# Performance work log

Hardware: AMD Instinct MI355X
Metric: run time of the kernel (lower is better)

Reference implementation:

```python
import jax, jax.numpy as jnp
import numpy as np

B, T, I, H, O, TGT = 64, 512, 64, 512, 64, 96
SCALE = 0.05


def setup_inputs() -> dict:
    key = jax.random.key(0)
    ks = jax.random.split(key, 12)
    rn = lambda k, sh: jax.random.normal(k, sh, jnp.float32) * SCALE
    return {
        "x": jax.random.normal(ks[0], (B, T, I), jnp.float32),
        "W_ih0": rn(ks[1], (4 * H, I)),
        "W_hh0": rn(ks[2], (4 * H, H)),
        "b_ih0": rn(ks[3], (4 * H,)),
        "b_hh0": rn(ks[4], (4 * H,)),
        "W_ih1": rn(ks[5], (4 * H, H)),
        "W_hh1": rn(ks[6], (4 * H, H)),
        "b_ih1": rn(ks[7], (4 * H,)),
        "b_hh1": rn(ks[8], (4 * H,)),
        "W_fc": rn(ks[9], (O, H)),
        "b_fc": rn(ks[10], (O,)),
        "target_len": TGT,
    }


def _cell(x_t, h, c, Wi, Wh, b):
    # PyTorch LSTM gate order: i, f, g, o
    g = x_t @ Wi.T + h @ Wh.T + b  # [B, 4H]
    i, f, gg, o = jnp.split(g, 4, axis=-1)
    c_new = jax.nn.sigmoid(f) * c + jax.nn.sigmoid(i) * jnp.tanh(gg)
    h_new = jax.nn.sigmoid(o) * jnp.tanh(c_new)
    return h_new, c_new


def _run_layer(seq_tbf, Wi, Wh, b):
    # seq_tbf: [T, B, F]; returns hidden sequence [T, B, H] and final (h, c)
    nb = seq_tbf.shape[1]
    hdim = Wh.shape[1]
    init = (jnp.zeros((nb, hdim), seq_tbf.dtype), jnp.zeros((nb, hdim), seq_tbf.dtype))

    def step(carry, x_t):
        h, c = _cell(x_t, carry[0], carry[1], Wi, Wh, b)
        return (h, c), h

    (h, c), hs = jax.lax.scan(step, init, seq_tbf)
    return hs, h, c


def reference(x, W_ih0, W_hh0, b_ih0, b_hh0, W_ih1, W_hh1, b_ih1, b_hh1, W_fc, b_fc, target_len):
    # Dropout is inactive (eval-mode reference).
    b0 = b_ih0 + b_hh0
    b1 = b_ih1 + b_hh1

    # --- encoder pass over full context ---
    seq = jnp.transpose(x, (1, 0, 2))                 # [T, B, I]
    hs0, h0, c0 = _run_layer(seq, W_ih0, W_hh0, b0)   # layer 0
    _, h1, c1 = _run_layer(hs0, W_ih1, W_hh1, b1)     # layer 1

    x_in = x[:, -1, :]  # [B, I]

    def dec_step(carry, _):
        h0, c0, h1, c1, xi = carry
        h0, c0 = _cell(xi, h0, c0, W_ih0, W_hh0, b0)
        h1, c1 = _cell(h0, h1, c1, W_ih1, W_hh1, b1)
        y = h1 @ W_fc.T + b_fc  # [B, O], fed back as next input
        return (h0, c0, h1, c1, y), y

    _, ys = jax.lax.scan(dec_step, (h0, c0, h1, c1, x_in), None, length=target_len)
    return jnp.transpose(ys, (1, 0, 2))  # [B, target_len, O]
```

## Files before the change

kernel.cpp:

```cpp
#include <hip/hip_runtime.h>
#include <stdint.h>


#define NWG 256
#define NTH 256

constexpr int Tt = 512, TGT = 96;

typedef __attribute__((ext_vector_type(8))) short bf16x8;
typedef __attribute__((ext_vector_type(4))) float f32x4;
typedef unsigned long long u64;

__device__ __forceinline__ unsigned short f2bf(float f) {
  union { float f; unsigned u; } v; v.f = f;
  return (unsigned short)((v.u + 0x7fffu + ((v.u >> 16) & 1u)) >> 16);
}
__device__ __forceinline__ float bf2f(unsigned short h) {
  union { unsigned u; float f; } v; v.u = ((unsigned)h) << 16; return v.f;
}
__device__ __forceinline__ float sigm(float x) { return 1.f / (1.f + __expf(-x)); }
__device__ __forceinline__ float tanh_(float x) { return 1.f - 2.f / (__expf(2.f * x) + 1.f); }

__device__ __forceinline__ unsigned ald32a(const unsigned* p) {
  return __hip_atomic_load(p, __ATOMIC_RELAXED, __HIP_MEMORY_SCOPE_AGENT);
}
__device__ __forceinline__ void ast32a(unsigned* p, unsigned v) {
  __hip_atomic_store(p, v, __ATOMIC_RELAXED, __HIP_MEMORY_SCOPE_AGENT);
}
__device__ __forceinline__ u64 ald64a(const u64* p) {
  return __hip_atomic_load(p, __ATOMIC_RELAXED, __HIP_MEMORY_SCOPE_AGENT);
}
__device__ __forceinline__ void ast64a(u64* p, u64 v) {
  __hip_atomic_store(p, v, __ATOMIC_RELAXED, __HIP_MEMORY_SCOPE_AGENT);
}

struct SMem {
  unsigned short wB[2][4][16][64][8];
  u64 a0[16 * 68];
  u64 a1[16 * 68];
  unsigned short wfc2[1024];
  float gpart[4][272];
  float fcp[256];
  float b0s[64], b1s[64], b0d[64], bfc2[2];
};

__device__ __forceinline__ int amap(int idx) {
  int b = idx >> 7, k8 = idx & 127;
  return (k8 >> 3) * 68 + b * 8 + (k8 & 7);
}

__device__ __forceinline__ void stage1(u64* dst, const u64* src, int tid) {
  u64 v0 = ald64a(src + tid),       v1 = ald64a(src + tid + 256);
  u64 v2 = ald64a(src + tid + 512), v3 = ald64a(src + tid + 768);
  dst[amap(tid)] = v0; dst[amap(tid + 256)] = v1;
  dst[amap(tid + 512)] = v2; dst[amap(tid + 768)] = v3;
}
__device__ __forceinline__ void stage2(u64* d0, const u64* s0, u64* d1, const u64* s1, int tid) {
  u64 v0 = ald64a(s0 + tid),       v1 = ald64a(s0 + tid + 256);
  u64 v2 = ald64a(s0 + tid + 512), v3 = ald64a(s0 + tid + 768);
  u64 v4 = ald64a(s1 + tid),       v5 = ald64a(s1 + tid + 256);
  u64 v6 = ald64a(s1 + tid + 512), v7 = ald64a(s1 + tid + 768);
  d0[amap(tid)] = v0; d0[amap(tid + 256)] = v1;
  d0[amap(tid + 512)] = v2; d0[amap(tid + 768)] = v3;
  d1[amap(tid)] = v4; d1[amap(tid + 256)] = v5;
  d1[amap(tid + 512)] = v6; d1[amap(tid + 768)] = v7;
}

__device__ __forceinline__ void gbar(unsigned* slots, int g, int w, unsigned tgt) {
  __syncthreads();
  if (threadIdx.x == 0) ast32a(slots + g * 32 + w, tgt);
  if (threadIdx.x < 64) {
    const unsigned* sp = slots + g * 32 + (threadIdx.x & 31);
    while (true) {
      unsigned v = ald32a(sp);
      if (__all((int)(v >= tgt))) break;
      __builtin_amdgcn_s_sleep(1);
    }
  }
  __syncthreads();
}

#define MFMA(a, b, c) __builtin_amdgcn_mfma_f32_16x16x32_bf16(a, b, c, 0, 0, 0)

__global__ __launch_bounds__(NTH, 1) void lstm_kernel(
    const float* __restrict__ x,
    const float* __restrict__ Wih0, const float* __restrict__ Whh0,
    const float* __restrict__ bih0, const float* __restrict__ bhh0,
    const float* __restrict__ Wih1, const float* __restrict__ Whh1,
    const float* __restrict__ bih1, const float* __restrict__ bhh1,
    const float* __restrict__ Wfc, const float* __restrict__ bfc,
    u64* h0q, u64* h1q, unsigned* slots, float* __restrict__ out)
{
  __shared__ SMem sm;
  const int g = blockIdx.x & 7;
  const int wgw = blockIdx.x >> 3;
  const int tid = threadIdx.x;

  for (int e = tid; e < 8192; e += NTH) {
    int m = e >> 12, w4 = (e >> 10) & 3, kc = (e >> 6) & 15, l = e & 63;
    int colx = l & 15, qx = l >> 4;
    size_t row = (size_t)((colx & 3) * 512 + wgw * 16 + w4 * 4 + (colx >> 2));
    const float* src = (m ? Wih1 : Whh0) + row * 512 + kc * 32 + qx * 8;
    unsigned short* dst = &sm.wB[m][w4][kc][l][0];
    float4 u = *(const float4*)src, v = *(const float4*)(src + 4);
    dst[0] = f2bf(u.x); dst[1] = f2bf(u.y); dst[2] = f2bf(u.z); dst[3] = f2bf(u.w);
    dst[4] = f2bf(v.x); dst[5] = f2bf(v.y); dst[6] = f2bf(v.z); dst[7] = f2bf(v.w);
  }
  for (int e = tid; e < 1024; e += NTH)
    sm.wfc2[e] = f2bf(Wfc[(size_t)(wgw * 2 + (e >> 9)) * 512 + (e & 511)]);
  if (tid < 64) {
    int jj = tid >> 2, g4 = tid & 3;
    int grow = g4 * 512 + wgw * 16 + jj;
    float s0 = bih0[grow] + bhh0[grow];
    sm.b0s[tid] = s0;
    sm.b1s[tid] = bih1[grow] + bhh1[grow];
    float ex = 0.f;
    for (int i = 0; i < 64; ++i) ex += Wih0[(size_t)grow * 64 + i] * bfc[i];
    sm.b0d[tid] = s0 + ex;
  }
  if (tid < 2) sm.bfc2[tid] = bfc[wgw * 2 + tid];

  const int wave = tid >> 6, lane = tid & 63;
  const int col = lane & 15, quad = lane >> 4;
  const int koff = quad * 8;
  const size_t rowg = (size_t)((col & 3) * 512 + wgw * 16 + wave * 4 + (col >> 2));

  bf16x8 whh1f[16];
#pragma unroll
  for (int kc = 0; kc < 16; ++kc) {
    const float* p = Whh1 + rowg * 512 + kc * 32 + koff;
    float4 u = *(const float4*)p, v = *(const float4*)(p + 4);
    bf16x8 r;
    r[0] = (short)f2bf(u.x); r[1] = (short)f2bf(u.y); r[2] = (short)f2bf(u.z); r[3] = (short)f2bf(u.w);
    r[4] = (short)f2bf(v.x); r[5] = (short)f2bf(v.y); r[6] = (short)f2bf(v.z); r[7] = (short)f2bf(v.w);
    whh1f[kc] = r;
  }
  bf16x8 wih0f[2];
#pragma unroll
  for (int kc = 0; kc < 2; ++kc) {
    const float* p = Wih0 + rowg * 64 + kc * 32 + koff;
    float4 u = *(const float4*)p, v = *(const float4*)(p + 4);
    bf16x8 r;
    r[0] = (short)f2bf(u.x); r[1] = (short)f2bf(u.y); r[2] = (short)f2bf(u.z); r[3] = (short)f2bf(u.w);
    r[4] = (short)f2bf(v.x); r[5] = (short)f2bf(v.y); r[6] = (short)f2bf(v.z); r[7] = (short)f2bf(v.w);
    wih0f[kc] = r;
  }
  bf16x8 wcombf[16];
  {
    float wc[16][8];
#pragma unroll
    for (int kc = 0; kc < 16; ++kc)
#pragma unroll
      for (int j = 0; j < 8; ++j) wc[kc][j] = 0.f;
    for (int i = 0; i < 64; ++i) {
      float wi = Wih0[rowg * 64 + i];
      const float* fr = Wfc + (size_t)i * 512 + koff;
#pragma unroll
      for (int kc = 0; kc < 16; ++kc) {
        float4 u = *(const float4*)(fr + kc * 32);
        float4 v = *(const float4*)(fr + kc * 32 + 4);
        wc[kc][0] += wi * u.x; wc[kc][1] += wi * u.y;
        wc[kc][2] += wi * u.z; wc[kc][3] += wi * u.w;
        wc[kc][4] += wi * v.x; wc[kc][5] += wi * v.y;
        wc[kc][6] += wi * v.z; wc[kc][7] += wi * v.w;
      }
    }
#pragma unroll
    for (int kc = 0; kc < 16; ++kc) {
      bf16x8 r;
#pragma unroll
      for (int j = 0; j < 8; ++j) r[j] = (short)f2bf(wc[kc][j]);
      wcombf[kc] = r;
    }
  }
  __syncthreads();

  const float b0c = sm.b0s[wave * 16 + col];
  const float b1c = sm.b1s[wave * 16 + col];
  const float b0dc = sm.b0d[wave * 16 + col];
  const unsigned short* pw0 = &sm.wB[0][wave][0][lane][0];
  const unsigned short* pw1 = &sm.wB[1][wave][0][lane][0];
  const u64* afrag0 = sm.a0 + (col & 7) * 8 + quad * 2;
  const u64* afrag1 = sm.a1 + (col & 7) * 8 + quad * 2;
  unsigned ph = 0;
  float c0 = 0.f, c1 = 0.f;
  const size_t xstride = (size_t)Tt * 64;

  auto loadx = [&](const float* p) -> bf16x8 {
    float4 u = *(const float4*)p, v = *(const float4*)(p + 4);
    bf16x8 r;
    r[0] = (short)f2bf(u.x); r[1] = (short)f2bf(u.y); r[2] = (short)f2bf(u.z); r[3] = (short)f2bf(u.w);
    r[4] = (short)f2bf(v.x); r[5] = (short)f2bf(v.y); r[6] = (short)f2bf(v.z); r[7] = (short)f2bf(v.w);
    return r;
  };

  auto actstore = [&](f32x4 v, float& cst, u64* hdst) {
    float* gp = sm.gpart[wave];
#pragma unroll
    for (int r = 0; r < 4; ++r) gp[(quad * 4 + r) * 17 + col] = v[r];
    unsigned hbits = 0;
    int b = lane >> 2, j = lane & 3;
    if (lane < 32) {
      const float* ro = gp + b * 17 + j * 4;
      float iv = sigm(ro[0]), fv = sigm(ro[1]), gv = tanh_(ro[2]), ov = sigm(ro[3]);
      float c = fv * cst + iv * gv; cst = c;
      hbits = f2bf(ov * tanh_(c));
    }
    unsigned h1b = __shfl(hbits, (lane + 1) & 63);
    unsigned h2b = __shfl(hbits, (lane + 2) & 63);
    unsigned h3b = __shfl(hbits, (lane + 3) & 63);
    if (lane < 32 && j == 0) {
      u64 pk = (u64)hbits | ((u64)h1b << 16) | ((u64)h2b << 32) | ((u64)h3b << 48);
      ast64a(hdst + b * 128 + wgw * 4 + wave, pk);
    }
  };

  auto fcpart = [&](const u64* asrc) {
    int ks = tid >> 4, b = (tid >> 1) & 7, cc = tid & 1;
    const unsigned short* hr = (const unsigned short*)(asrc + ks * 68 + b * 8);
    const unsigned short* wp = sm.wfc2 + cc * 512 + ks * 32;
    float s = 0.f;
#pragma unroll
    for (int k2 = 0; k2 < 4; ++k2) {
      bf16x8 hv = *(const bf16x8*)(hr + k2 * 8);
      bf16x8 wv = *(const bf16x8*)(wp + k2 * 8);
#pragma unroll
      for (int q2 = 0; q2 < 8; ++q2) s += bf2f((unsigned short)hv[q2]) * bf2f((unsigned short)wv[q2]);
    }
    sm.fcp[tid] = s;
  };
  auto fcout = [&](int d) {
    if (tid < 16) {
      float sv = sm.bfc2[tid & 1];
#pragma unroll
      for (int k = 0; k < 16; ++k) sv += sm.fcp[k * 16 + tid];
      int bb = tid >> 1, cc = tid & 1;
      out[(size_t)(g * 8 + bb) * (TGT * 64) + d * 64 + (wgw * 2 + cc)] = sv;
    }
  };

  for (int t = 0; t <= Tt; ++t) {
    const u64* h0prev = h0q + ((t + 1) & 1) * 8192 + g * 1024;
    u64* h0cur = h0q + (t & 1) * 8192 + g * 1024;
    const u64* h1prev = h1q + (t & 1) * 8192 + g * 1024;
    u64* h1cur = h1q + ((t + 1) & 1) * 8192 + g * 1024;

    bf16x8 xa0, xa1;
    if (t < Tt) {
      const float* xb = x + (size_t)(g * 8 + (col & 7)) * xstride + (size_t)t * 64 + koff;
      xa0 = loadx(xb); xa1 = loadx(xb + 32);
    }
    if (t == 1)      { stage1(sm.a0, h0prev, tid); __syncthreads(); }
    else if (t >= 2) { stage2(sm.a0, h0prev, sm.a1, h1prev, tid); __syncthreads(); }

    if (t < Tt) {
      f32x4 za = {b0c, b0c, b0c, b0c}, zb = {0.f, 0.f, 0.f, 0.f};
      za = MFMA(xa0, wih0f[0], za);
      zb = MFMA(xa1, wih0f[1], zb);
      if (t >= 1) {
        f32x4 ya = {b1c, b1c, b1c, b1c}, yb = {0.f, 0.f, 0.f, 0.f};
#pragma unroll
        for (int kc = 0; kc < 16; ++kc) {
          bf16x8 a = *(const bf16x8*)(afrag0 + kc * 68);
          bf16x8 w0 = *(const bf16x8*)(pw0 + kc * 512);
          bf16x8 w1 = *(const bf16x8*)(pw1 + kc * 512);
          if (kc & 1) { zb = MFMA(a, w0, zb); yb = MFMA(a, w1, yb); }
          else        { za = MFMA(a, w0, za); ya = MFMA(a, w1, ya); }
        }
        if (t >= 2) {
#pragma unroll
          for (int kc = 0; kc < 16; ++kc) {
            bf16x8 a = *(const bf16x8*)(afrag1 + kc * 68);
            if (kc & 1) yb = MFMA(a, whh1f[kc], yb);
            else        ya = MFMA(a, whh1f[kc], ya);
          }
        }
        actstore(za + zb, c0, h0cur);
        actstore(ya + yb, c1, h1cur);
      } else {
        actstore(za + zb, c0, h0cur);
      }
    } else {
      f32x4 ya = {b1c, b1c, b1c, b1c}, yb = {0.f, 0.f, 0.f, 0.f};
#pragma unroll
      for (int kc = 0; kc < 16; ++kc) {
        bf16x8 a = *(const bf16x8*)(afrag0 + kc * 68);
        bf16x8 w1 = *(const bf16x8*)(pw1 + kc * 512);
        if (kc & 1) yb = MFMA(a, w1, yb);
        else        ya = MFMA(a, w1, ya);
      }
#pragma unroll
      for (int kc = 0; kc < 16; ++kc) {
        bf16x8 a = *(const bf16x8*)(afrag1 + kc * 68);
        if (kc & 1) yb = MFMA(a, whh1f[kc], yb);
        else        ya = MFMA(a, whh1f[kc], ya);
      }
      actstore(ya + yb, c1, h1cur);
    }
    gbar(slots, g, wgw, ++ph);
  }

  {
    stage2(sm.a0, h0q + 8192 + g * 1024, sm.a1, h1q + 8192 + g * 1024, tid);
    __syncthreads();
    const float* xb = x + (size_t)(g * 8 + (col & 7)) * xstride + (size_t)(Tt - 1) * 64 + koff;
    bf16x8 xa0 = loadx(xb), xa1 = loadx(xb + 32);
    f32x4 za = {b0c, b0c, b0c, b0c}, zb = {0.f, 0.f, 0.f, 0.f};
    za = MFMA(xa0, wih0f[0], za);
    zb = MFMA(xa1, wih0f[1], zb);
#pragma unroll
    for (int kc = 0; kc < 16; ++kc) {
      bf16x8 a = *(const bf16x8*)(afrag0 + kc * 68);
      bf16x8 w0 = *(const bf16x8*)(pw0 + kc * 512);
      if (kc & 1) zb = MFMA(a, w0, zb);
      else        za = MFMA(a, w0, za);
    }
    actstore(za + zb, c0, h0q + g * 1024);
  }
  gbar(slots, g, wgw, ++ph);
  {
    stage1(sm.a0, h0q + g * 1024, tid);
    __syncthreads();
    f32x4 ya = {b1c, b1c, b1c, b1c}, yb = {0.f, 0.f, 0.f, 0.f};
#pragma unroll
    for (int kc = 0; kc < 16; ++kc) {
      bf16x8 a = *(const bf16x8*)(afrag0 + kc * 68);
      bf16x8 w1 = *(const bf16x8*)(pw1 + kc * 512);
      bf16x8 a2 = *(const bf16x8*)(afrag1 + kc * 68);
      if (kc & 1) { yb = MFMA(a, w1, yb); yb = MFMA(a2, whh1f[kc], yb); }
      else        { ya = MFMA(a, w1, ya); ya = MFMA(a2, whh1f[kc], ya); }
    }
    actstore(ya + yb, c1, h1q + g * 1024);
  }
  gbar(slots, g, wgw, ++ph);

  for (int d = 1; d < TGT; ++d) {
    {
      stage2(sm.a0, h0q + ((d + 1) & 1) * 8192 + g * 1024,
             sm.a1, h1q + ((d + 1) & 1) * 8192 + g * 1024, tid);
      __syncthreads();
      fcpart(sm.a1);
      f32x4 za = {b0dc, b0dc, b0dc, b0dc}, zb = {0.f, 0.f, 0.f, 0.f};
#pragma unroll
      for (int kc = 0; kc < 16; ++kc) {
        bf16x8 a = *(const bf16x8*)(afrag0 + kc * 68);
        bf16x8 w0 = *(const bf16x8*)(pw0 + kc * 512);
        bf16x8 a2 = *(const bf16x8*)(afrag1 + kc * 68);
        if (kc & 1) { zb = MFMA(a, w0, zb); zb = MFMA(a2, wcombf[kc], zb); }
        else        { za = MFMA(a, w0, za); za = MFMA(a2, wcombf[kc], za); }
      }
      actstore(za + zb, c0, h0q + (d & 1) * 8192 + g * 1024);
      __syncthreads();
      fcout(d - 1);
    }
    gbar(slots, g, wgw, ++ph);

    {
      stage1(sm.a0, h0q + (d & 1) * 8192 + g * 1024, tid);
      __syncthreads();
      f32x4 ya = {b1c, b1c, b1c, b1c}, yb = {0.f, 0.f, 0.f, 0.f};
#pragma unroll
      for (int kc = 0; kc < 16; ++kc) {
        bf16x8 a = *(const bf16x8*)(afrag0 + kc * 68);
        bf16x8 w1 = *(const bf16x8*)(pw1 + kc * 512);
        bf16x8 a2 = *(const bf16x8*)(afrag1 + kc * 68);
        if (kc & 1) { yb = MFMA(a, w1, yb); yb = MFMA(a2, whh1f[kc], yb); }
        else        { ya = MFMA(a, w1, ya); ya = MFMA(a2, whh1f[kc], ya); }
      }
      actstore(ya + yb, c1, h1q + (d & 1) * 8192 + g * 1024);
    }
    gbar(slots, g, wgw, ++ph);
  }

  {
    stage1(sm.a1, h1q + 8192 + g * 1024, tid);
    __syncthreads();
    fcpart(sm.a1);
    __syncthreads();
    fcout(TGT - 1);
  }
}

extern "C" void kernel_launch(void* const* d_in, const int* in_sizes, int n_in,
                              void* d_out, int out_size, void* d_ws, size_t ws_size,
                              hipStream_t stream) {
  (void)in_sizes; (void)n_in; (void)out_size; (void)ws_size;
  const float* x    = (const float*)d_in[0];
  const float* Wih0 = (const float*)d_in[1];
  const float* Whh0 = (const float*)d_in[2];
  const float* bih0 = (const float*)d_in[3];
  const float* bhh0 = (const float*)d_in[4];
  const float* Wih1 = (const float*)d_in[5];
  const float* Whh1 = (const float*)d_in[6];
  const float* bih1 = (const float*)d_in[7];
  const float* bhh1 = (const float*)d_in[8];
  const float* Wfc  = (const float*)d_in[9];
  const float* bfc  = (const float*)d_in[10];

  char* ws = (char*)d_ws;
  unsigned* slots = (unsigned*)ws;
  u64* h0q = (u64*)(ws + 2048);
  u64* h1q = (u64*)(ws + 2048 + 131072);

  hipMemsetAsync(slots, 0, 2048, stream);
  hipLaunchKernelGGL(lstm_kernel, dim3(NWG), dim3(NTH), 0, stream,
                     x, Wih0, Whh0, bih0, bhh0, Wih1, Whh1, bih1, bhh1, Wfc, bfc,
                     h0q, h1q, slots, (float*)d_out);
}
```

Before: 2.898 ms.

## Replace per-step global barriers with tag-bit polling on hidden-state data

Drops the slot-counter barrier that ran after every LSTM step. Each packed bf16 hidden value now carries an epoch-parity tag in its exponent MSB, and consumers spin on the data itself until every tag matches before staging it into LDS. This removes a separate flag write plus polling round trip per step and lets workgroups wait only on the data they actually need. The trade-off is that it relies on |h|<2 so the tag bit is otherwise zero, and a bounded retry guard could let stale data through if a producer is very late.

```diff
diff --git a/kernel.cpp b/kernel.cpp
--- a/kernel.cpp
+++ b/kernel.cpp
@@ -11,6 +11,8 @@
 typedef __attribute__((ext_vector_type(4))) float f32x4;
 typedef unsigned long long u64;
 
+#define TAGBITS 0x4000400040004000ULL
+
 __device__ __forceinline__ unsigned short f2bf(float f) {
   union { float f; unsigned u; } v; v.f = f;
   return (unsigned short)((v.u + 0x7fffu + ((v.u >> 16) & 1u)) >> 16);
@@ -21,17 +23,17 @@
 __device__ __forceinline__ float sigm(float x) { return 1.f / (1.f + __expf(-x)); }
 __device__ __forceinline__ float tanh_(float x) { return 1.f - 2.f / (__expf(2.f * x) + 1.f); }
 
-__device__ __forceinline__ unsigned ald32a(const unsigned* p) {
-  return __hip_atomic_load(p, __ATOMIC_RELAXED, __HIP_MEMORY_SCOPE_AGENT);
-}
-__device__ __forceinline__ void ast32a(unsigned* p, unsigned v) {
-  __hip_atomic_store(p, v, __ATOMIC_RELAXED, __HIP_MEMORY_SCOPE_AGENT);
-}
 __device__ __forceinline__ u64 ald64a(const u64* p) {
   return __hip_atomic_load(p, __ATOMIC_RELAXED, __HIP_MEMORY_SCOPE_AGENT);
 }
 __device__ __forceinline__ void ast64a(u64* p, u64 v) {
   __hip_atomic_store(p, v, __ATOMIC_RELAXED, __HIP_MEMORY_SCOPE_AGENT);
+}
+
+__device__ __forceinline__ u64 tmask(int e) {
+  int q = (e >> 1) & 3;
+  return (u64)(q & 1) * 0x0000400000004000ULL
+       | (u64)((q >> 1) & 1) * 0x4000000040000000ULL;
 }
 
 struct SMem {
@@ -49,35 +51,40 @@
   return (k8 >> 3) * 68 + b * 8 + (k8 & 7);
 }
 
-__device__ __forceinline__ void stage1(u64* dst, const u64* src, int tid) {
-  u64 v0 = ald64a(src + tid),       v1 = ald64a(src + tid + 256);
-  u64 v2 = ald64a(src + tid + 512), v3 = ald64a(src + tid + 768);
-  dst[amap(tid)] = v0; dst[amap(tid + 256)] = v1;
-  dst[amap(tid + 512)] = v2; dst[amap(tid + 768)] = v3;
-}
-__device__ __forceinline__ void stage2(u64* d0, const u64* s0, u64* d1, const u64* s1, int tid) {
-  u64 v0 = ald64a(s0 + tid),       v1 = ald64a(s0 + tid + 256);
-  u64 v2 = ald64a(s0 + tid + 512), v3 = ald64a(s0 + tid + 768);
-  u64 v4 = ald64a(s1 + tid),       v5 = ald64a(s1 + tid + 256);
-  u64 v6 = ald64a(s1 + tid + 512), v7 = ald64a(s1 + tid + 768);
-  d0[amap(tid)] = v0; d0[amap(tid + 256)] = v1;
-  d0[amap(tid + 512)] = v2; d0[amap(tid + 768)] = v3;
-  d1[amap(tid)] = v4; d1[amap(tid + 256)] = v5;
-  d1[amap(tid + 512)] = v6; d1[amap(tid + 768)] = v7;
-}
-
-__device__ __forceinline__ void gbar(unsigned* slots, int g, int w, unsigned tgt) {
-  __syncthreads();
-  if (threadIdx.x == 0) ast32a(slots + g * 32 + w, tgt);
-  if (threadIdx.x < 64) {
-    const unsigned* sp = slots + g * 32 + (threadIdx.x & 31);
-    while (true) {
-      unsigned v = ald32a(sp);
-      if (__all((int)(v >= tgt))) break;
-      __builtin_amdgcn_s_sleep(1);
-    }
-  }
-  __syncthreads();
+__device__ __forceinline__ void pollstage1(u64* dst, const u64* src, u64 want, int tid) {
+  u64 v0, v1, v2, v3;
+  int guard = 0;
+  while (true) {
+    v0 = ald64a(src + tid);       v1 = ald64a(src + tid + 256);
+    v2 = ald64a(src + tid + 512); v3 = ald64a(src + tid + 768);
+    bool ok = ((v0 & TAGBITS) == want) & ((v1 & TAGBITS) == want) &
+              ((v2 & TAGBITS) == want) & ((v3 & TAGBITS) == want);
+    if (ok || ++guard > 8192) break;
+    __builtin_amdgcn_s_sleep(1);
+  }
+  dst[amap(tid)]       = v0 & ~TAGBITS; dst[amap(tid + 256)] = v1 & ~TAGBITS;
+  dst[amap(tid + 512)] = v2 & ~TAGBITS; dst[amap(tid + 768)] = v3 & ~TAGBITS;
+}
+__device__ __forceinline__ void pollstage2(u64* d0, const u64* s0, u64 w0,
+                                           u64* d1, const u64* s1, u64 w1, int tid) {
+  u64 a0, a1, a2, a3, b0, b1, b2, b3;
+  int guard = 0;
+  while (true) {
+    a0 = ald64a(s0 + tid);       a1 = ald64a(s0 + tid + 256);
+    a2 = ald64a(s0 + tid + 512); a3 = ald64a(s0 + tid + 768);
+    b0 = ald64a(s1 + tid);       b1 = ald64a(s1 + tid + 256);
+    b2 = ald64a(s1 + tid + 512); b3 = ald64a(s1 + tid + 768);
+    bool ok = ((a0 & TAGBITS) == w0) & ((a1 & TAGBITS) == w0) &
+              ((a2 & TAGBITS) == w0) & ((a3 & TAGBITS) == w0) &
+              ((b0 & TAGBITS) == w1) & ((b1 & TAGBITS) == w1) &
+              ((b2 & TAGBITS) == w1) & ((b3 & TAGBITS) == w1);
+    if (ok || ++guard > 8192) break;
+    __builtin_amdgcn_s_sleep(1);
+  }
+  d0[amap(tid)]       = a0 & ~TAGBITS; d0[amap(tid + 256)] = a1 & ~TAGBITS;
+  d0[amap(tid + 512)] = a2 & ~TAGBITS; d0[amap(tid + 768)] = a3 & ~TAGBITS;
+  d1[amap(tid)]       = b0 & ~TAGBITS; d1[amap(tid + 256)] = b1 & ~TAGBITS;
+  d1[amap(tid + 512)] = b2 & ~TAGBITS; d1[amap(tid + 768)] = b3 & ~TAGBITS;
 }
 
 #define MFMA(a, b, c) __builtin_amdgcn_mfma_f32_16x16x32_bf16(a, b, c, 0, 0, 0)
@@ -89,7 +96,7 @@
     const float* __restrict__ Wih1, const float* __restrict__ Whh1,
     const float* __restrict__ bih1, const float* __restrict__ bhh1,
     const float* __restrict__ Wfc, const float* __restrict__ bfc,
-    u64* h0q, u64* h1q, unsigned* slots, float* __restrict__ out)
+    u64* h0q, u64* h1q, float* __restrict__ out)
 {
   __shared__ SMem sm;
   const int g = blockIdx.x & 7;
@@ -182,9 +189,12 @@
   const unsigned short* pw1 = &sm.wB[1][wave][0][lane][0];
   const u64* afrag0 = sm.a0 + (col & 7) * 8 + quad * 2;
   const u64* afrag1 = sm.a1 + (col & 7) * 8 + quad * 2;
-  unsigned ph = 0;
   float c0 = 0.f, c1 = 0.f;
   const size_t xstride = (size_t)Tt * 64;
+
+  auto hslot = [&](u64* hq, int e) -> u64* {
+    return hq + ((size_t)(e & 1) << 13) + g * 1024;
+  };
 
   auto loadx = [&](const float* p) -> bf16x8 {
     float4 u = *(const float4*)p, v = *(const float4*)(p + 4);
@@ -194,7 +204,7 @@
     return r;
   };
 
-  auto actstore = [&](f32x4 v, float& cst, u64* hdst) {
+  auto actstore = [&](f32x4 v, float& cst, u64* hdst, u64 tg) {
     float* gp = sm.gpart[wave];
 #pragma unroll
     for (int r = 0; r < 4; ++r) gp[(quad * 4 + r) * 17 + col] = v[r];
@@ -211,7 +221,7 @@
     unsigned h3b = __shfl(hbits, (lane + 3) & 63);
     if (lane < 32 && j == 0) {
       u64 pk = (u64)hbits | ((u64)h1b << 16) | ((u64)h2b << 32) | ((u64)h3b << 48);
-      ast64a(hdst + b * 128 + wgw * 4 + wave, pk);
+      ast64a(hdst + b * 128 + wgw * 4 + wave, pk | tg);
     }
   };
 
@@ -240,18 +250,21 @@
   };
 
   for (int t = 0; t <= Tt; ++t) {
-    const u64* h0prev = h0q + ((t + 1) & 1) * 8192 + g * 1024;
-    u64* h0cur = h0q + (t & 1) * 8192 + g * 1024;
-    const u64* h1prev = h1q + (t & 1) * 8192 + g * 1024;
-    u64* h1cur = h1q + ((t + 1) & 1) * 8192 + g * 1024;
-
     bf16x8 xa0, xa1;
     if (t < Tt) {
       const float* xb = x + (size_t)(g * 8 + (col & 7)) * xstride + (size_t)t * 64 + koff;
       xa0 = loadx(xb); xa1 = loadx(xb + 32);
     }
-    if (t == 1)      { stage1(sm.a0, h0prev, tid); __syncthreads(); }
-    else if (t >= 2) { stage2(sm.a0, h0prev, sm.a1, h1prev, tid); __syncthreads(); }
+    if (t == 1) {
+      __syncthreads();
+      pollstage1(sm.a0, hslot(h0q, 0), tmask(0), tid);
+      __syncthreads();
+    } else if (t >= 2) {
+      __syncthreads();
+      pollstage2(sm.a0, hslot(h0q, t - 1), tmask(t - 1),
+                 sm.a1, hslot(h1q, t - 2), tmask(t - 2), tid);
+      __syncthreads();
+    }
 
     if (t < Tt) {
       f32x4 za = {b0c, b0c, b0c, b0c}, zb = {0.f, 0.f, 0.f, 0.f};
@@ -275,10 +288,10 @@
             else        ya = MFMA(a, whh1f[kc], ya);
           }
         }
-        actstore(za + zb, c0, h0cur);
-        actstore(ya + yb, c1, h1cur);
+        actstore(za + zb, c0, hslot(h0q, t), tmask(t));
+        actstore(ya + yb, c1, hslot(h1q, t - 1), tmask(t - 1));
       } else {
-        actstore(za + zb, c0, h0cur);
+        actstore(za + zb, c0, hslot(h0q, 0), tmask(0));
       }
     } else {
       f32x4 ya = {b1c, b1c, b1c, b1c}, yb = {0.f, 0.f, 0.f, 0.f};
@@ -295,13 +308,14 @@
         if (kc & 1) yb = MFMA(a, whh1f[kc], yb);
         else        ya = MFMA(a, whh1f[kc], ya);
       }
-      actstore(ya + yb, c1, h1cur);
-    }
-    gbar(slots, g, wgw, ++ph);
+      actstore(ya + yb, c1, hslot(h1q, Tt - 1), tmask(Tt - 1));
+    }
   }
 
   {
-    stage2(sm.a0, h0q + 8192 + g * 1024, sm.a1, h1q + 8192 + g * 1024, tid);
+    __syncthreads();
+    pollstage2(sm.a0, hslot(h0q, 511), tmask(511),
+               sm.a1, hslot(h1q, 511), tmask(511), tid);
     __syncthreads();
     const float* xb = x + (size_t)(g * 8 + (col & 7)) * xstride + (size_t)(Tt - 1) * 64 + koff;
     bf16x8 xa0 = loadx(xb), xa1 = loadx(xb + 32);
@@ -315,11 +329,11 @@
       if (kc & 1) zb = MFMA(a, w0, zb);
       else        za = MFMA(a, w0, za);
     }
-    actstore(za + zb, c0, h0q + g * 1024);
-  }
-  gbar(slots, g, wgw, ++ph);
+    actstore(za + zb, c0, hslot(h0q, 512), tmask(512));
+  }
   {
-    stage1(sm.a0, h0q + g * 1024, tid);
+    __syncthreads();
+    pollstage1(sm.a0, hslot(h0q, 512), tmask(512), tid);
     __syncthreads();
     f32x4 ya = {b1c, b1c, b1c, b1c}, yb = {0.f, 0.f, 0.f, 0.f};
 #pragma unroll
@@ -330,14 +344,14 @@
       if (kc & 1) { yb = MFMA(a, w1, yb); yb = MFMA(a2, whh1f[kc], yb); }
       else        { ya = MFMA(a, w1, ya); ya = MFMA(a2, whh1f[kc], ya); }
     }
-    actstore(ya + yb, c1, h1q + g * 1024);
-  }
-  gbar(slots, g, wgw, ++ph);
+    actstore(ya + yb, c1, hslot(h1q, 512), tmask(512));
+  }
 
   for (int d = 1; d < TGT; ++d) {
     {
-      stage2(sm.a0, h0q + ((d + 1) & 1) * 8192 + g * 1024,
-             sm.a1, h1q + ((d + 1) & 1) * 8192 + g * 1024, tid);
+      __syncthreads();
+      pollstage2(sm.a0, hslot(h0q, 511 + d), tmask(511 + d),
+                 sm.a1, hslot(h1q, 511 + d), tmask(511 + d), tid);
       __syncthreads();
       fcpart(sm.a1);
       f32x4 za = {b0dc, b0dc, b0dc, b0dc}, zb = {0.f, 0.f, 0.f, 0.f};
@@ -349,14 +363,13 @@
         if (kc & 1) { zb = MFMA(a, w0, zb); zb = MFMA(a2, wcombf[kc], zb); }
         else        { za = MFMA(a, w0, za); za = MFMA(a2, wcombf[kc], za); }
       }
-      actstore(za + zb, c0, h0q + (d & 1) * 8192 + g * 1024);
+      actstore(za + zb, c0, hslot(h0q, 512 + d), tmask(512 + d));
       __syncthreads();
       fcout(d - 1);
     }
-    gbar(slots, g, wgw, ++ph);
-
     {
-      stage1(sm.a0, h0q + (d & 1) * 8192 + g * 1024, tid);
+      __syncthreads();
+      pollstage1(sm.a0, hslot(h0q, 512 + d), tmask(512 + d), tid);
       __syncthreads();
       f32x4 ya = {b1c, b1c, b1c, b1c}, yb = {0.f, 0.f, 0.f, 0.f};
 #pragma unroll
@@ -367,13 +380,13 @@
         if (kc & 1) { yb = MFMA(a, w1, yb); yb = MFMA(a2, whh1f[kc], yb); }
         else        { ya = MFMA(a, w1, ya); ya = MFMA(a2, whh1f[kc], ya); }
       }
-      actstore(ya + yb, c1, h1q + (d & 1) * 8192 + g * 1024);
-    }
-    gbar(slots, g, wgw, ++ph);
+      actstore(ya + yb, c1, hslot(h1q, 512 + d), tmask(512 + d));
+    }
   }
 
   {
-    stage1(sm.a1, h1q + 8192 + g * 1024, tid);
+    __syncthreads();
+    pollstage1(sm.a1, hslot(h1q, 512 + TGT - 1), tmask(512 + TGT - 1), tid);
     __syncthreads();
     fcpart(sm.a1);
     __syncthreads();
@@ -398,12 +411,11 @@
   const float* bfc  = (const float*)d_in[10];
 
   char* ws = (char*)d_ws;
-  unsigned* slots = (unsigned*)ws;
-  u64* h0q = (u64*)(ws + 2048);
-  u64* h1q = (u64*)(ws + 2048 + 131072);
-
-  hipMemsetAsync(slots, 0, 2048, stream);
+  u64* h0q = (u64*)ws;
+  u64* h1q = (u64*)(ws + 131072);
+
+  hipMemsetAsync(ws, 0xFF, 262144, stream);
   hipLaunchKernelGGL(lstm_kernel, dim3(NWG), dim3(NTH), 0, stream,
                      x, Wih0, Whh0, bih0, bhh0, Wih1, Whh1, bih1, bhh1, Wfc, bfc,
-                     h0q, h1q, slots, (float*)d_out);
-}
+                     h0q, h1q, (float*)d_out);
+}
```

New measurement: 2.940 ms. Within noise of the previous version (+1.5%).
